# Optimization experiments

Measured on AMD Instinct MI355X. Metric: run time of the kernel, lower is better.

The kernel has to match this reference:

```python
import jax, jax.numpy as jnp
import numpy as np

L, D, H, M, NC = 12, 768, 12, 3072, 1000
P, IMG, C = 16, 224, 3
HD = D // H // 2  # 32: diff-attn head dim (2*H query heads of HD, H value heads of 2*HD)
B = 32
N = (IMG // P) ** 2 + 1  # 197
EPS = 1e-5


def _layernorm(x, s, b):
    mu = x.mean(-1, keepdims=True)
    var = ((x - mu) ** 2).mean(-1, keepdims=True)
    return (x - mu) * jax.lax.rsqrt(var + EPS) * s + b


def _rmsnorm(x, s):
    ms = (x * x).mean(-1, keepdims=True)
    return x * jax.lax.rsqrt(ms + EPS) * s


def _diff_attn(x, qw, kw, vw, ow, lq1, lk1, lq2, lk2, sls, lam_init):
    b, n, _ = x.shape
    q = (x @ qw).reshape(b, n, 2 * H, HD)
    k = (x @ kw).reshape(b, n, 2 * H, HD)
    v = (x @ vw).reshape(b, n, H, 2 * HD)
    scores = jnp.einsum('bnhd,bmhd->bhnm', q, k) * (HD ** -0.5)
    attn = jax.nn.softmax(scores, axis=-1)  # [b, 2H, n, n]
    lam = jnp.exp(jnp.sum(lq1 * lk1)) - jnp.exp(jnp.sum(lq2 * lk2)) + lam_init
    attn = attn.reshape(b, H, 2, n, n)
    attn = attn[:, :, 0] - lam * attn[:, :, 1]  # differential attention map
    out = jnp.einsum('bhnm,bmhd->bnhd', attn, v)  # [b, n, H, 2*HD]
    out = _rmsnorm(out, sls) * (1.0 - lam_init)
    return out.reshape(b, n, D) @ ow


def _forward(x, conv_w, conv_b, cls_token, pos_emb,
             ln1_s, ln1_b, q_w, k_w, v_w, o_w, lq1, lk1, lq2, lk2, subln_s,
             ln2_s, ln2_b, w1, b1, w2, b2, lnf_s, lnf_b, head_w, head_b):
    # patch embed: conv stride=patch, then flatten to tokens
    h = jax.lax.conv_general_dilated(x, conv_w, (P, P), 'VALID',
                                     dimension_numbers=('NCHW', 'OIHW', 'NCHW'))
    h = h + conv_b[None, :, None, None]
    bsz = x.shape[0]
    h = h.reshape(bsz, D, -1).transpose(0, 2, 1)  # [B, 196, D]
    h = jnp.concatenate([jnp.broadcast_to(cls_token, (bsz, 1, D)), h], axis=1)
    h = h + pos_emb
    for i in range(L):
        lam_init = 0.8 - 0.6 * np.exp(-0.3 * i)
        a = _diff_attn(_layernorm(h, ln1_s[i], ln1_b[i]), q_w[i], k_w[i], v_w[i], o_w[i],
                       lq1[i], lk1[i], lq2[i], lk2[i], subln_s[i], lam_init)
        h = h + a
        m = _layernorm(h, ln2_s[i], ln2_b[i])
        m = jax.nn.gelu(m @ w1[i] + b1[i]) @ w2[i] + b2[i]
        h = h + m
    h = _layernorm(h, lnf_s, lnf_b)
    return h[:, 0] @ head_w + head_b


def setup_inputs() -> dict:
    key = jax.random.key(0)
    ks = iter(jax.random.split(key, 40))
    def rn(shape, s=0.02):
        return jax.random.normal(next(ks), shape, jnp.float32) * s
    return {
        'x': jax.random.normal(next(ks), (B, C, IMG, IMG), jnp.float32),
        'conv_w': rn((D, C, P, P)), 'conv_b': jnp.zeros((D,), jnp.float32),
        'cls_token': jnp.zeros((1, 1, D), jnp.float32),
        'pos_emb': rn((1, N, D)),
        'ln1_s': jnp.ones((L, D), jnp.float32), 'ln1_b': jnp.zeros((L, D), jnp.float32),
        'q_w': rn((L, D, D)), 'k_w': rn((L, D, D)), 'v_w': rn((L, D, D)), 'o_w': rn((L, D, D)),
        'lq1': rn((L, HD), 0.1), 'lk1': rn((L, HD), 0.1),
        'lq2': rn((L, HD), 0.1), 'lk2': rn((L, HD), 0.1),
        'subln_s': jnp.ones((L, 2 * HD), jnp.float32),
        'ln2_s': jnp.ones((L, D), jnp.float32), 'ln2_b': jnp.zeros((L, D), jnp.float32),
        'w1': rn((L, D, M)), 'b1': jnp.zeros((L, M), jnp.float32),
        'w2': rn((L, M, D)), 'b2': jnp.zeros((L, D), jnp.float32),
        'lnf_s': jnp.ones((D,), jnp.float32), 'lnf_b': jnp.zeros((D,), jnp.float32),
        'head_w': rn((D, NC)), 'head_b': jnp.zeros((NC,), jnp.float32),
    }


def reference(x, conv_w, conv_b, cls_token, pos_emb,
              ln1_s, ln1_b, q_w, k_w, v_w, o_w, lq1, lk1, lq2, lk2, subln_s,
              ln2_s, ln2_b, w1, b1, w2, b2, lnf_s, lnf_b, head_w, head_b):
    return _forward(x, conv_w, conv_b, cls_token, pos_emb,
                    ln1_s, ln1_b, q_w, k_w, v_w, o_w, lq1, lk1, lq2, lk2, subln_s,
                    ln2_s, ln2_b, w1, b1, w2, b2, lnf_s, lnf_b, head_w, head_b)
```

## Files before the change

### kernel.cpp

```cpp
#include <hip/hip_runtime.h>
#include <cmath>


typedef unsigned short u16;
typedef u16 u16x4 __attribute__((ext_vector_type(4)));
typedef u16 u16x8 __attribute__((ext_vector_type(8)));
typedef float fx4 __attribute__((ext_vector_type(4)));
typedef __bf16 bf16x8 __attribute__((ext_vector_type(8)));

#define MROWS 6304
#define MPAD  6400

#define WAITV(N) asm volatile("s_waitcnt vmcnt(" #N ")" ::: "memory")

__device__ __forceinline__ float bf2f(u16 u) {
  union { unsigned int i; float f; } c; c.i = ((unsigned int)u) << 16; return c.f;
}
__device__ __forceinline__ u16 f2bf(float f) {
  union { float f; unsigned int i; } c; c.f = f;
  return (u16)((c.i + 0x7FFFu + ((c.i >> 16) & 1u)) >> 16);
}
__device__ __forceinline__ float gelu_f(float x) {
  float u = 0.7978845608028654f * (x + 0.044715f * x * x * x);
  u = fminf(fmaxf(u, -30.f), 30.f);
  float e = __expf(2.f * u);
  return 0.5f * x * (1.f + (e - 1.f) / (e + 1.f));
}

__device__ __forceinline__ void gload16(const void* g, void* l) {
  __builtin_amdgcn_global_load_lds(
      (const __attribute__((address_space(1))) void*)g,
      (__attribute__((address_space(3))) void*)l, 16, 0, 0);
}

__device__ __forceinline__ int xcd_swz(int orig, int nwg) {
  int q = nwg >> 3, r = nwg & 7;
  int x = orig & 7, i = orig >> 3;
  return (x < r ? x * (q + 1) : r * (q + 1) + (x - r) * q) + i;
}

enum { EP_F32 = 0, EP_BF16 = 1, EP_GELU_BF16 = 2, EP_RESID_F32 = 3 };

template<int MODE>
__device__ __forceinline__ void ep_store(void* outp, const float* __restrict__ resid,
                                         size_t m, size_t n, size_t N, float v) {
  if (MODE == EP_GELU_BF16)      ((u16*)outp)[m * N + n] = f2bf(gelu_f(v));
  else if (MODE == EP_BF16)      ((u16*)outp)[m * N + n] = f2bf(v);
  else if (MODE == EP_RESID_F32) ((float*)outp)[m * N + n] = resid[m * N + n] + v;
  else                           ((float*)outp)[m * N + n] = v;
}

template<int MODE, bool BIAS>
__device__ __forceinline__
void gemm_256_body(const u16* __restrict__ A, const u16* __restrict__ Bt,
                   const float* __restrict__ bias, const float* __restrict__ resid,
                   void* __restrict__ outp, int M, int N, int K, int NT)
{
  extern __shared__ unsigned char lds[];
  const int tid = threadIdx.x;
  const int lane = tid & 63, w = tid >> 6;
  const int g = lane >> 4, l = lane & 15;
  const int wr = w >> 2, wc = w & 3;
  const int wg = xcd_swz(blockIdx.x, gridDim.x);
  const int bm = (wg / NT) * 256, bn = (wg % NT) * 256;
  const int NKT = K >> 6;

  const int srow = w * 16 + (lane >> 3);
  const int scol = ((lane & 7) ^ ((lane >> 3) & 7)) << 3;
  const u16* gA = A + (size_t)bm * K + scol;
  const u16* gB = Bt + (size_t)bn * K + scol;
  const int ldso = (w * 16) * 128;

  auto STG = [&](int buf, int op, int half, int t) {
    const u16* src = (op ? gB : gA) + (size_t)(half * 128 + srow) * K + t * 64;
    unsigned char* d = lds + buf * 65536 + op * 32768 + half * 16384 + ldso;
    gload16(src, d);
    gload16(src + (size_t)8 * K, d + 1024);
  };

  fx4 acc[2][2][4][2] = {};

  STG(0, 0, 0, 0); STG(0, 1, 0, 0); STG(0, 0, 1, 0); STG(0, 1, 1, 0);
  STG(1, 0, 0, 1); STG(1, 1, 0, 1);
  WAITV(4);
  __builtin_amdgcn_s_barrier();

  for (int T = 0; T < NKT; ++T) {
    const unsigned char* Ab = lds + (T & 1) * 65536;
    const unsigned char* Bb = Ab + 32768;

#define RD_A(i2, kk, mh) (*(const bf16x8*)(Ab + ((mh)*128 + wr*64 + (i2)*16 + l)*128 + (((kk)*64 + g*16) ^ ((l & 7) << 4))))
#define RD_B(j2, kk, nh) (*(const bf16x8*)(Bb + ((nh)*128 + wc*32 + (j2)*16 + l)*128 + (((kk)*64 + g*16) ^ ((l & 7) << 4))))
#define PHASE(mh, nh, DOWAIT, ...)                                             \
    {                                                                          \
      bf16x8 af0[4], af1[4], bq0[2], bq1[2];                                   \
      _Pragma("unroll") for (int i2 = 0; i2 < 4; ++i2) {                       \
        af0[i2] = RD_A(i2, 0, mh); af1[i2] = RD_A(i2, 1, mh);                  \
      }                                                                        \
      _Pragma("unroll") for (int j2 = 0; j2 < 2; ++j2) {                       \
        bq0[j2] = RD_B(j2, 0, nh); bq1[j2] = RD_B(j2, 1, nh);                  \
      }                                                                        \
      __VA_ARGS__;                                                             \
      if (DOWAIT) WAITV(4);                                                    \
      __builtin_amdgcn_s_barrier();                                            \
      asm volatile("s_waitcnt lgkmcnt(0)" ::: "memory");                       \
      __builtin_amdgcn_sched_barrier(0);                                       \
      __builtin_amdgcn_s_setprio(1);                                           \
      _Pragma("unroll") for (int i2 = 0; i2 < 4; ++i2)                         \
        _Pragma("unroll") for (int j2 = 0; j2 < 2; ++j2) {                     \
          acc[mh][nh][i2][j2] = __builtin_amdgcn_mfma_f32_16x16x32_bf16(       \
              af0[i2], bq0[j2], acc[mh][nh][i2][j2], 0, 0, 0);                 \
          acc[mh][nh][i2][j2] = __builtin_amdgcn_mfma_f32_16x16x32_bf16(       \
              af1[i2], bq1[j2], acc[mh][nh][i2][j2], 0, 0, 0);                 \
        }                                                                      \
      __builtin_amdgcn_s_setprio(0);                                           \
      __builtin_amdgcn_s_barrier();                                            \
    }

    PHASE(0, 0, false, { if (T + 1 < NKT) STG((T + 1) & 1, 0, 1, T + 1); })
    PHASE(0, 1, false, { if (T + 1 < NKT) STG((T + 1) & 1, 1, 1, T + 1); })
    PHASE(1, 0, false, { if (T + 2 < NKT) STG(T & 1, 0, 0, T + 2); })
    PHASE(1, 1, true,  { if (T + 2 < NKT) STG(T & 1, 1, 0, T + 2); })

#undef PHASE
#undef RD_A
#undef RD_B
  }

  #pragma unroll
  for (int mh = 0; mh < 2; ++mh)
    #pragma unroll
    for (int i2 = 0; i2 < 4; ++i2)
      #pragma unroll
      for (int qr = 0; qr < 4; ++qr) {
        int m = bm + mh * 128 + wr * 64 + i2 * 16 + g * 4 + qr;
        if (m < M) {
          #pragma unroll
          for (int nh = 0; nh < 2; ++nh)
            #pragma unroll
            for (int j2 = 0; j2 < 2; ++j2) {
              int n = bn + nh * 128 + wc * 32 + j2 * 16 + l;
              float bv = BIAS ? bias[n] : 0.f;
              ep_store<MODE>(outp, resid, m, n, N, acc[mh][nh][i2][j2][qr] + bv);
            }
        }
      }
}

template<int MODE, bool BIAS>
__device__ __forceinline__
void gemm_n64_body(const u16* __restrict__ A, const u16* __restrict__ Bt,
                   const float* __restrict__ bias, const float* __restrict__ resid,
                   void* __restrict__ outp, int M, int N, int K, int NT)
{
  __shared__ unsigned char lds[2][(128 + 64) * 64 * 2];
  const int tid = threadIdx.x;
  const int lane = tid & 63, w = tid >> 6;
  const int g = lane >> 4, l = lane & 15;
  const int wg = xcd_swz(blockIdx.x, gridDim.x);
  const int bm = (wg / NT) * 128, bn = (wg % NT) * 64;

  const int swz_half = ((lane & 7) ^ ((lane >> 3) & 7)) << 3;
  const u16* gA = A + (size_t)(bm + 32 * w + (lane >> 3)) * K + swz_half;
  const u16* gB = Bt + (size_t)(bn + 16 * w + (lane >> 3)) * K + swz_half;

  fx4 acc[2][4] = {};

  auto STAGE = [&](int buf, int kt) {
    unsigned char* bA = &lds[buf][0] + 4096 * w;
    unsigned char* bB = &lds[buf][0] + 16384 + 2048 * w;
    #pragma unroll
    for (int c = 0; c < 4; ++c)
      gload16(gA + (size_t)(8 * c) * K + kt, bA + (8 * c) * 128);
    #pragma unroll
    for (int c = 0; c < 2; ++c)
      gload16(gB + (size_t)(8 * c) * K + kt, bB + (8 * c) * 128);
  };

  STAGE(0, 0);
  int cur = 0;
  for (int kt = 0; kt < K; kt += 64) {
    if (kt + 64 < K) {
      STAGE(cur ^ 1, kt + 64);
      WAITV(6);
    } else {
      WAITV(0);
    }
    __builtin_amdgcn_s_barrier();
    __builtin_amdgcn_sched_barrier(0);
    const unsigned char* As = &lds[cur][0];
    const unsigned char* Bs = As + 16384;
    #pragma unroll
    for (int kk = 0; kk < 2; ++kk) {
      bf16x8 af[2], bfr[4];
      #pragma unroll
      for (int i = 0; i < 2; ++i) {
        int ar = w * 32 + i * 16 + l;
        af[i] = *(const bf16x8*)(As + ar * 128 + ((kk * 64 + g * 16) ^ ((ar & 7) << 4)));
      }
      #pragma unroll
      for (int j = 0; j < 4; ++j) {
        int br = j * 16 + l;
        bfr[j] = *(const bf16x8*)(Bs + br * 128 + ((kk * 64 + g * 16) ^ ((br & 7) << 4)));
      }
      #pragma unroll
      for (int i = 0; i < 2; ++i)
        #pragma unroll
        for (int j = 0; j < 4; ++j)
          acc[i][j] = __builtin_amdgcn_mfma_f32_16x16x32_bf16(af[i], bfr[j], acc[i][j], 0, 0, 0);
    }
    __builtin_amdgcn_sched_barrier(0);
    __builtin_amdgcn_s_barrier();
    cur ^= 1;
  }
  #pragma unroll
  for (int j = 0; j < 4; ++j) {
    int n = bn + j * 16 + l;
    float bv = BIAS ? bias[n] : 0.f;
    #pragma unroll
    for (int i = 0; i < 2; ++i) {
      int mbase = bm + w * 32 + i * 16 + g * 4;
      #pragma unroll
      for (int q = 0; q < 4; ++q) {
        int m = mbase + q;
        if (m < M) ep_store<MODE>(outp, resid, m, n, N, acc[i][j][q] + bv);
      }
    }
  }
}

__global__ __launch_bounds__(256) void patch_gemm(const u16* A, const u16* Bt, float* outp) {
  gemm_n64_body<EP_F32, false>(A, Bt, nullptr, nullptr, outp, 6272, 768, 768, 12);
}
__global__ __launch_bounds__(512) void qkv_gemm(const u16* A, const u16* Bt, u16* outp) {
  gemm_256_body<EP_BF16, false>(A, Bt, nullptr, nullptr, outp, MROWS, 2304, 768, 9);
}
__global__ __launch_bounds__(256) void oproj_gemm(const u16* A, const u16* Bt,
                                                  const float* resid, float* outp) {
  gemm_n64_body<EP_RESID_F32, false>(A, Bt, nullptr, resid, outp, MROWS, 768, 768, 12);
}
__global__ __launch_bounds__(512) void mlp1_gemm(const u16* A, const u16* Bt,
                                                 const float* bias, u16* outp) {
  gemm_256_body<EP_GELU_BF16, true>(A, Bt, bias, nullptr, outp, MROWS, 3072, 768, 12);
}
__global__ __launch_bounds__(256) void mlp2_gemm(const u16* A, const u16* Bt,
                                                 const float* bias, const float* resid,
                                                 float* outp) {
  gemm_n64_body<EP_RESID_F32, true>(A, Bt, bias, resid, outp, MROWS, 768, 3072, 12);
}

template<bool OUTF32>
__global__ __launch_bounds__(64)
void layernorm_k(const float* __restrict__ x, const float* __restrict__ s,
                 const float* __restrict__ b, void* __restrict__ outp, size_t in_rstride)
{
  int r = blockIdx.x, lane = threadIdx.x;
  const fx4* xp = (const fx4*)(x + (size_t)r * in_rstride);
  fx4 v[3];
  float sum = 0.f, sq = 0.f;
  #pragma unroll
  for (int j = 0; j < 3; ++j) {
    v[j] = xp[j * 64 + lane];
    #pragma unroll
    for (int e = 0; e < 4; ++e) { sum += v[j][e]; sq += v[j][e] * v[j][e]; }
  }
  #pragma unroll
  for (int off = 32; off; off >>= 1) { sum += __shfl_xor(sum, off); sq += __shfl_xor(sq, off); }
  float mu = sum * (1.f / 768.f);
  float var = sq * (1.f / 768.f) - mu * mu;
  float rs = rsqrtf(var + 1e-5f);
  const fx4* sp = (const fx4*)s;
  const fx4* bp = (const fx4*)b;
  #pragma unroll
  for (int j = 0; j < 3; ++j) {
    fx4 sv = sp[j * 64 + lane], bv = bp[j * 64 + lane];
    if (OUTF32) {
      fx4 o;
      #pragma unroll
      for (int e = 0; e < 4; ++e) o[e] = (v[j][e] - mu) * rs * sv[e] + bv[e];
      *(fx4*)((float*)outp + (size_t)r * 768 + (j * 64 + lane) * 4) = o;
    } else {
      u16x4 o;
      #pragma unroll
      for (int e = 0; e < 4; ++e) o[e] = f2bf((v[j][e] - mu) * rs * sv[e] + bv[e]);
      *(u16x4*)((u16*)outp + (size_t)r * 768 + (j * 64 + lane) * 4) = o;
    }
  }
}

#define KSTR 40
#define VSTR 232
#define DA_LDS (2 * 224 * KSTR * 2 + 64 * VSTR * 2 + 4 * 16 * VSTR * 2)

__global__ __launch_bounds__(256)
void diff_attn(const u16* __restrict__ qkv, const float* __restrict__ lam_p,
               const float* __restrict__ sls, u16* __restrict__ outp, float lam_init)
{
  extern __shared__ char smem[];
  u16* K1s = (u16*)smem;
  u16* K2s = K1s + 224 * KSTR;
  u16* Vt  = K2s + 224 * KSTR;
  const int tid = threadIdx.x;
  const int w = tid >> 6, lane = tid & 63;
  const int g = lane >> 4, l = lane & 15;
  u16* Pw = Vt + 64 * VSTR + w * 16 * VSTR;

  const int bh = blockIdx.x;
  const int b = bh / 12, hh = bh % 12;
  const u16* base = qkv + (size_t)b * 197 * 2304;

  if (tid < 197) {
    const u16* kr = base + (size_t)tid * 2304 + 768 + hh * 64;
    *(u16x8*)(K1s + tid * KSTR + 0)  = *(const u16x8*)(kr + 0);
    *(u16x8*)(K1s + tid * KSTR + 8)  = *(const u16x8*)(kr + 8);
    *(u16x8*)(K1s + tid * KSTR + 16) = *(const u16x8*)(kr + 16);
    *(u16x8*)(K1s + tid * KSTR + 24) = *(const u16x8*)(kr + 24);
    *(u16x8*)(K2s + tid * KSTR + 0)  = *(const u16x8*)(kr + 32);
    *(u16x8*)(K2s + tid * KSTR + 8)  = *(const u16x8*)(kr + 40);
    *(u16x8*)(K2s + tid * KSTR + 16) = *(const u16x8*)(kr + 48);
    *(u16x8*)(K2s + tid * KSTR + 24) = *(const u16x8*)(kr + 56);
    const u16* vr = base + (size_t)tid * 2304 + 1536 + hh * 64;
    #pragma unroll
    for (int jj = 0; jj < 8; ++jj) {
      u16x8 vv = *(const u16x8*)(vr + jj * 8);
      #pragma unroll
      for (int e = 0; e < 8; ++e) Vt[(jj * 8 + e) * VSTR + tid] = vv[e];
    }
  }
  for (int idx = tid; idx < 64 * 27; idx += 256) {
    Vt[(idx / 27) * VSTR + 197 + (idx % 27)] = 0;
  }
  __syncthreads();

  const float lam = lam_p[0];
  const float oscale = 1.f - lam_init;
  const float scale = 0.17677669529663687f;
  const fx4 zero = {};

  for (int qb = w; qb < 13; qb += 4) {
    const int qbase = qb * 16;
    const u16* qrow = base + (size_t)(qbase + l) * 2304 + hh * 64;
    bf16x8 qf1 = *(const bf16x8*)(qrow + g * 8);
    bf16x8 qf2 = *(const bf16x8*)(qrow + 32 + g * 8);

    fx4 s1[14], s2[14];
    #pragma unroll
    for (int t = 0; t < 14; ++t) {
      bf16x8 kf1 = *(const bf16x8*)(K1s + (t * 16 + l) * KSTR + g * 8);
      bf16x8 kf2 = *(const bf16x8*)(K2s + (t * 16 + l) * KSTR + g * 8);
      s1[t] = __builtin_amdgcn_mfma_f32_16x16x32_bf16(qf1, kf1, zero, 0, 0, 0);
      s2[t] = __builtin_amdgcn_mfma_f32_16x16x32_bf16(qf2, kf2, zero, 0, 0, 0);
    }

    float mx1[4] = {-1e30f, -1e30f, -1e30f, -1e30f};
    float mx2[4] = {-1e30f, -1e30f, -1e30f, -1e30f};
    #pragma unroll
    for (int t = 0; t < 14; ++t) {
      bool ok = (t * 16 + l) < 197;
      #pragma unroll
      for (int q = 0; q < 4; ++q) {
        float v1 = ok ? s1[t][q] * scale : -1e30f;
        float v2 = ok ? s2[t][q] * scale : -1e30f;
        s1[t][q] = v1; s2[t][q] = v2;
        mx1[q] = fmaxf(mx1[q], v1); mx2[q] = fmaxf(mx2[q], v2);
      }
    }
    #pragma unroll
    for (int off = 8; off; off >>= 1)
      #pragma unroll
      for (int q = 0; q < 4; ++q) {
        mx1[q] = fmaxf(mx1[q], __shfl_xor(mx1[q], off));
        mx2[q] = fmaxf(mx2[q], __shfl_xor(mx2[q], off));
      }
    float z1[4] = {0, 0, 0, 0}, z2[4] = {0, 0, 0, 0};
    #pragma unroll
    for (int t = 0; t < 14; ++t)
      #pragma unroll
      for (int q = 0; q < 4; ++q) {
        float p1 = __expf(s1[t][q] - mx1[q]);
        float p2 = __expf(s2[t][q] - mx2[q]);
        s1[t][q] = p1; s2[t][q] = p2;
        z1[q] += p1; z2[q] += p2;
      }
    #pragma unroll
    for (int off = 8; off; off >>= 1)
      #pragma unroll
      for (int q = 0; q < 4; ++q) {
        z1[q] += __shfl_xor(z1[q], off);
        z2[q] += __shfl_xor(z2[q], off);
      }
    float r1[4], r2[4];
    #pragma unroll
    for (int q = 0; q < 4; ++q) { r1[q] = 1.f / z1[q]; r2[q] = lam / z2[q]; }

    #pragma unroll
    for (int t = 0; t < 14; ++t)
      #pragma unroll
      for (int q = 0; q < 4; ++q) {
        float pc = s1[t][q] * r1[q] - s2[t][q] * r2[q];
        Pw[(g * 4 + q) * VSTR + t * 16 + l] = f2bf(pc);
      }

    fx4 o[4] = {};
    #pragma unroll
    for (int mt = 0; mt < 7; ++mt) {
      bf16x8 pa = *(const bf16x8*)(Pw + l * VSTR + mt * 32 + g * 8);
      #pragma unroll
      for (int j = 0; j < 4; ++j) {
        bf16x8 vb = *(const bf16x8*)(Vt + (j * 16 + l) * VSTR + mt * 32 + g * 8);
        o[j] = __builtin_amdgcn_mfma_f32_16x16x32_bf16(pa, vb, o[j], 0, 0, 0);
      }
    }

    float ms[4] = {0, 0, 0, 0};
    #pragma unroll
    for (int j = 0; j < 4; ++j)
      #pragma unroll
      for (int q = 0; q < 4; ++q) ms[q] += o[j][q] * o[j][q];
    #pragma unroll
    for (int off = 8; off; off >>= 1)
      #pragma unroll
      for (int q = 0; q < 4; ++q) ms[q] += __shfl_xor(ms[q], off);
    float rr[4];
    #pragma unroll
    for (int q = 0; q < 4; ++q) rr[q] = rsqrtf(ms[q] * (1.f / 64.f) + 1e-5f) * oscale;
    #pragma unroll
    for (int j = 0; j < 4; ++j) {
      float slv = sls[j * 16 + l];
      #pragma unroll
      for (int q = 0; q < 4; ++q) {
        int row = qbase + g * 4 + q;
        if (row < 197)
          outp[(size_t)(b * 197 + row) * 768 + hh * 64 + j * 16 + l] = f2bf(o[j][q] * rr[q] * slv);
      }
    }
  }
}

__global__ __launch_bounds__(256)
void prep_weights(const float* __restrict__ qw, const float* __restrict__ kw,
                  const float* __restrict__ vw, const float* __restrict__ ow,
                  const float* __restrict__ w1, const float* __restrict__ w2,
                  u16* __restrict__ qkvt, u16* __restrict__ ot,
                  u16* __restrict__ w1t, u16* __restrict__ w2t,
                  const float* __restrict__ lq1, const float* __restrict__ lk1,
                  const float* __restrict__ lq2, const float* __restrict__ lk2,
                  float* __restrict__ lam_out, float lam_init)
{
  int bid = blockIdx.x;
  if (bid == 1728) {
    if (threadIdx.x < 64) {
      int lane = threadIdx.x;
      float p1 = lane < 32 ? lq1[lane] * lk1[lane] : 0.f;
      float p2 = lane < 32 ? lq2[lane] * lk2[lane] : 0.f;
      #pragma unroll
      for (int off = 32; off; off >>= 1) { p1 += __shfl_xor(p1, off); p2 += __shfl_xor(p2, off); }
      if (lane == 0) lam_out[0] = __expf(p1) - __expf(p2) + lam_init;
    }
    return;
  }
  const float* src; u16* dst; int Kd, Nd, tx, ty;
  if (bid < 576) {
    int which = bid / 144, t = bid % 144;
    ty = t / 12; tx = t % 12; Kd = 768; Nd = 768;
    src = (which == 0) ? qw : (which == 1) ? kw : (which == 2) ? vw : ow;
    dst = (which < 3) ? (qkvt + (size_t)which * 768 * 768) : ot;
  } else if (bid < 1152) {
    int t = bid - 576; ty = t / 12; tx = t % 12; Kd = 768; Nd = 3072; src = w1; dst = w1t;
  } else {
    int t = bid - 1152; ty = t / 48; tx = t % 48; Kd = 3072; Nd = 768; src = w2; dst = w2t;
  }
  __shared__ u16 tile[64][65];
  int tid2 = threadIdx.x;
  int k0 = tx * 64, n0 = ty * 64;
  #pragma unroll
  for (int j = 0; j < 16; ++j) {
    int idx = j * 256 + tid2;
    int rr = idx >> 6, cc = idx & 63;
    tile[rr][cc] = f2bf(src[(size_t)(k0 + rr) * Nd + n0 + cc]);
  }
  __syncthreads();
  #pragma unroll
  for (int j = 0; j < 16; ++j) {
    int idx = j * 256 + tid2;
    int rr = idx >> 6, cc = idx & 63;
    dst[(size_t)(n0 + rr) * Kd + k0 + cc] = tile[cc][rr];
  }
}

__global__ void convert_cw(const float* __restrict__ src, u16* __restrict__ dst)
{
  int i4 = blockIdx.x * 256 + threadIdx.x;
  fx4 v = *(const fx4*)(src + (size_t)i4 * 4);
  u16x4 o;
  #pragma unroll
  for (int e = 0; e < 4; ++e) o[e] = f2bf(v[e]);
  *(u16x4*)(dst + (size_t)i4 * 4) = o;
}

__global__ void im2col(const float* __restrict__ x, u16* __restrict__ A0)
{
  int i4 = blockIdx.x * 256 + threadIdx.x;
  int base = i4 * 4;
  int r = base / 768, c0 = base % 768;
  int b = r / 196, p = r % 196;
  int py = p / 14, px = p % 14;
  int ch = c0 >> 8;
  int cc = c0 & 255;
  int iy = cc >> 4, ix = cc & 15;
  const float* src = x + (((size_t)(b * 3 + ch) * 224 + py * 16 + iy) * 224 + px * 16 + ix);
  fx4 v = *(const fx4*)src;
  u16x4 o;
  #pragma unroll
  for (int e = 0; e < 4; ++e) o[e] = f2bf(v[e]);
  *(u16x4*)(A0 + base) = o;
}

__global__ void assemble(const float* __restrict__ tmp, const float* __restrict__ conv_b,
                         const float* __restrict__ cls, const float* __restrict__ pos,
                         float* __restrict__ h)
{
  int i4 = blockIdx.x * 256 + threadIdx.x;
  int base = i4 * 4;
  int r = base / 768, d = base % 768;
  int b = r / 197, n = r % 197;
  fx4 pv = *(const fx4*)(pos + (size_t)n * 768 + d);
  fx4 v;
  if (n == 0) {
    v = *(const fx4*)(cls + d);
  } else {
    v = *(const fx4*)(tmp + (size_t)(b * 196 + n - 1) * 768 + d);
    fx4 cb = *(const fx4*)(conv_b + d);
    v = v + cb;
  }
  *(fx4*)(h + (size_t)r * 768 + d) = v + pv;
}

__global__ __launch_bounds__(256)
void head_kernel(const float* __restrict__ ln, const float* __restrict__ hw,
                 const float* __restrict__ hb, float* __restrict__ outp)
{
  int r = blockIdx.x;
  int c = blockIdx.y * 256 + threadIdx.x;
  if (c >= 1000) return;
  const float* lr = ln + (size_t)r * 768;
  float acc = hb[c];
  for (int d = 0; d < 768; ++d)
    acc = fmaf(lr[d], hw[(size_t)d * 1000 + c], acc);
  outp[r * 1000 + c] = acc;
}

extern "C" void kernel_launch(void* const* d_in, const int* in_sizes, int n_in,
                              void* d_out, int out_size, void* d_ws, size_t ws_size,
                              hipStream_t stream)
{
  (void)in_sizes; (void)n_in; (void)out_size; (void)ws_size;
  const float* x      = (const float*)d_in[0];
  const float* conv_w = (const float*)d_in[1];
  const float* conv_b = (const float*)d_in[2];
  const float* cls    = (const float*)d_in[3];
  const float* pos    = (const float*)d_in[4];
  const float* ln1_s  = (const float*)d_in[5];
  const float* ln1_b  = (const float*)d_in[6];
  const float* q_w    = (const float*)d_in[7];
  const float* k_w    = (const float*)d_in[8];
  const float* v_w    = (const float*)d_in[9];
  const float* o_w    = (const float*)d_in[10];
  const float* lq1    = (const float*)d_in[11];
  const float* lk1    = (const float*)d_in[12];
  const float* lq2    = (const float*)d_in[13];
  const float* lk2    = (const float*)d_in[14];
  const float* slsx   = (const float*)d_in[15];
  const float* ln2_s  = (const float*)d_in[16];
  const float* ln2_b  = (const float*)d_in[17];
  const float* w1     = (const float*)d_in[18];
  const float* b1     = (const float*)d_in[19];
  const float* w2     = (const float*)d_in[20];
  const float* b2     = (const float*)d_in[21];
  const float* lnf_s  = (const float*)d_in[22];
  const float* lnf_b  = (const float*)d_in[23];
  const float* head_w = (const float*)d_in[24];
  const float* head_b = (const float*)d_in[25];
  float* out = (float*)d_out;

  char* ws = (char*)d_ws;
  size_t off = 0;
  auto alloc = [&](size_t bytes) { size_t p = off; off += (bytes + 255) & ~(size_t)255; return p; };
  u16*   A_bf  = (u16*)  (ws + alloc((size_t)MPAD * 768 * 2));
  u16*   big   = (u16*)  (ws + alloc((size_t)MPAD * 3072 * 2));
  float* h     = (float*)(ws + alloc((size_t)MROWS * 768 * 4));
  u16*   wqkv  = (u16*)  (ws + alloc((size_t)2304 * 768 * 2));
  u16*   wo    = (u16*)  (ws + alloc((size_t)768 * 768 * 2));
  u16*   w1t   = (u16*)  (ws + alloc((size_t)3072 * 768 * 2));
  u16*   w2t   = (u16*)  (ws + alloc((size_t)768 * 3072 * 2));
  float* lnf_o = (float*)(ws + alloc((size_t)32 * 768 * 4));
  float* lam   = (float*)(ws + alloc(256));
  float* convtmp = (float*)big;
  u16*   cwbf  = w1t;

  hipFuncSetAttribute((const void*)diff_attn,
                      hipFuncAttributeMaxDynamicSharedMemorySize, DA_LDS);
  hipFuncSetAttribute((const void*)qkv_gemm,
                      hipFuncAttributeMaxDynamicSharedMemorySize, 131072);
  hipFuncSetAttribute((const void*)mlp1_gemm,
                      hipFuncAttributeMaxDynamicSharedMemorySize, 131072);

  convert_cw<<<576, 256, 0, stream>>>(conv_w, cwbf);
  im2col<<<4704, 256, 0, stream>>>(x, A_bf);
  patch_gemm<<<588, 256, 0, stream>>>(A_bf, cwbf, convtmp);
  assemble<<<4728, 256, 0, stream>>>(convtmp, conv_b, cls, pos, h);

  for (int l = 0; l < 12; ++l) {
    float lam_init = 0.8f - 0.6f * expf(-0.3f * (float)l);
    prep_weights<<<1729, 256, 0, stream>>>(
        q_w + (size_t)l * 589824, k_w + (size_t)l * 589824,
        v_w + (size_t)l * 589824, o_w + (size_t)l * 589824,
        w1 + (size_t)l * 2359296, w2 + (size_t)l * 2359296,
        wqkv, wo, w1t, w2t,
        lq1 + l * 32, lk1 + l * 32, lq2 + l * 32, lk2 + l * 32,
        lam, lam_init);
    layernorm_k<false><<<MROWS, 64, 0, stream>>>(h, ln1_s + l * 768, ln1_b + l * 768, A_bf, (size_t)768);
    qkv_gemm<<<225, 512, 131072, stream>>>(A_bf, wqkv, big);
    diff_attn<<<384, 256, DA_LDS, stream>>>(big, lam, slsx + l * 64, A_bf, lam_init);
    oproj_gemm<<<600, 256, 0, stream>>>(A_bf, wo, h, h);
    layernorm_k<false><<<MROWS, 64, 0, stream>>>(h, ln2_s + l * 768, ln2_b + l * 768, A_bf, (size_t)768);
    mlp1_gemm<<<300, 512, 131072, stream>>>(A_bf, w1t, b1 + l * 3072, big);
    mlp2_gemm<<<600, 256, 0, stream>>>(big, w2t, b2 + l * 768, h, h);
  }

  layernorm_k<true><<<32, 64, 0, stream>>>(h, lnf_s, lnf_b, lnf_o, (size_t)197 * 768);
  head_kernel<<<dim3(32, 4), 256, 0, stream>>>(lnf_o, head_w, head_b, out);
}
```

Before: 3.136 ms.

## Triple-buffer N64 GEMM loads and retile MLP1 into 128x128 blocks

The N=64 GEMM body (patch, o-proj, mlp2) moves from a double-buffered static LDS pipeline to a triple-buffered one in dynamic LDS, so loads run two k-tiles ahead with matching vmcnt waits. MLP1 drops the 256x256, 512-thread kernel for a new 128x128, 256-thread tiled kernel launched over 1200 workgroups. The aim is to hide global-load latency better and raise occupancy and grid balance for MLP1. In exchange, the smaller MLP1 tiles get less reuse per workgroup, and the N64 kernels use more LDS per workgroup.

```diff
diff --git a/kernel.cpp b/kernel.cpp
--- a/kernel.cpp
+++ b/kernel.cpp
@@ -149,16 +149,97 @@
 
 template<int MODE, bool BIAS>
 __device__ __forceinline__
+void gemm_big_body(const u16* __restrict__ A, const u16* __restrict__ Bt,
+                   const float* __restrict__ bias, const float* __restrict__ resid,
+                   void* __restrict__ outp, int M, int N, int K, int NT)
+{
+  __shared__ unsigned char lds[2][2 * 128 * 64 * 2];
+  const int tid = threadIdx.x;
+  const int lane = tid & 63, w = tid >> 6;
+  const int g = lane >> 4, l = lane & 15;
+  const int wr = w >> 1, wc = w & 1;
+  const int wg = xcd_swz(blockIdx.x, gridDim.x);
+  const int bm = (wg / NT) * 128, bn = (wg % NT) * 128;
+
+  const int swz_half = ((lane & 7) ^ ((lane >> 3) & 7)) << 3;
+  const int srow = 32 * w + (lane >> 3);
+  const u16* gA = A + (size_t)(bm + srow) * K + swz_half;
+  const u16* gB = Bt + (size_t)(bn + srow) * K + swz_half;
+
+  fx4 acc[4][4] = {};
+
+  auto STAGE = [&](int buf, int kt) {
+    unsigned char* bA = &lds[buf][0] + 4096 * w;
+    unsigned char* bB = bA + 16384;
+    #pragma unroll
+    for (int c = 0; c < 4; ++c) {
+      gload16(gA + (size_t)(8 * c) * K + kt, bA + (8 * c) * 128);
+      gload16(gB + (size_t)(8 * c) * K + kt, bB + (8 * c) * 128);
+    }
+  };
+
+  STAGE(0, 0);
+  int cur = 0;
+  for (int kt = 0; kt < K; kt += 64) {
+    if (kt + 64 < K) {
+      STAGE(cur ^ 1, kt + 64);
+      WAITV(8);
+    } else {
+      WAITV(0);
+    }
+    __builtin_amdgcn_s_barrier();
+    __builtin_amdgcn_sched_barrier(0);
+    const unsigned char* As = &lds[cur][0];
+    const unsigned char* Bs = As + 16384;
+    #pragma unroll
+    for (int kk = 0; kk < 2; ++kk) {
+      bf16x8 af[4], bfr[4];
+      #pragma unroll
+      for (int i = 0; i < 4; ++i) {
+        int ar = wr * 64 + i * 16 + l;
+        af[i] = *(const bf16x8*)(As + ar * 128 + ((kk * 64 + g * 16) ^ ((ar & 7) << 4)));
+        int br = wc * 64 + i * 16 + l;
+        bfr[i] = *(const bf16x8*)(Bs + br * 128 + ((kk * 64 + g * 16) ^ ((br & 7) << 4)));
+      }
+      #pragma unroll
+      for (int i = 0; i < 4; ++i)
+        #pragma unroll
+        for (int j = 0; j < 4; ++j)
+          acc[i][j] = __builtin_amdgcn_mfma_f32_16x16x32_bf16(af[i], bfr[j], acc[i][j], 0, 0, 0);
+    }
+    __builtin_amdgcn_sched_barrier(0);
+    __builtin_amdgcn_s_barrier();
+    cur ^= 1;
+  }
+  #pragma unroll
+  for (int j = 0; j < 4; ++j) {
+    int n = bn + wc * 64 + j * 16 + l;
+    float bv = BIAS ? bias[n] : 0.f;
+    #pragma unroll
+    for (int i = 0; i < 4; ++i) {
+      int mbase = bm + wr * 64 + i * 16 + g * 4;
+      #pragma unroll
+      for (int q = 0; q < 4; ++q) {
+        int m = mbase + q;
+        if (m < M) ep_store<MODE>(outp, resid, m, n, N, acc[i][j][q] + bv);
+      }
+    }
+  }
+}
+
+template<int MODE, bool BIAS>
+__device__ __forceinline__
 void gemm_n64_body(const u16* __restrict__ A, const u16* __restrict__ Bt,
                    const float* __restrict__ bias, const float* __restrict__ resid,
                    void* __restrict__ outp, int M, int N, int K, int NT)
 {
-  __shared__ unsigned char lds[2][(128 + 64) * 64 * 2];
+  extern __shared__ unsigned char lds3[];
   const int tid = threadIdx.x;
   const int lane = tid & 63, w = tid >> 6;
   const int g = lane >> 4, l = lane & 15;
   const int wg = xcd_swz(blockIdx.x, gridDim.x);
   const int bm = (wg / NT) * 128, bn = (wg % NT) * 64;
+  const int NKT = K >> 6;
 
   const int swz_half = ((lane & 7) ^ ((lane >> 3) & 7)) << 3;
   const u16* gA = A + (size_t)(bm + 32 * w + (lane >> 3)) * K + swz_half;
@@ -166,29 +247,32 @@
 
   fx4 acc[2][4] = {};
 
-  auto STAGE = [&](int buf, int kt) {
-    unsigned char* bA = &lds[buf][0] + 4096 * w;
-    unsigned char* bB = &lds[buf][0] + 16384 + 2048 * w;
+  auto STAGE = [&](int buf, int t) {
+    unsigned char* bA = lds3 + buf * 24576 + 4096 * w;
+    unsigned char* bB = lds3 + buf * 24576 + 16384 + 2048 * w;
     #pragma unroll
     for (int c = 0; c < 4; ++c)
-      gload16(gA + (size_t)(8 * c) * K + kt, bA + (8 * c) * 128);
+      gload16(gA + (size_t)(8 * c) * K + t * 64, bA + (8 * c) * 128);
     #pragma unroll
     for (int c = 0; c < 2; ++c)
-      gload16(gB + (size_t)(8 * c) * K + kt, bB + (8 * c) * 128);
+      gload16(gB + (size_t)(8 * c) * K + t * 64, bB + (8 * c) * 128);
   };
 
   STAGE(0, 0);
-  int cur = 0;
-  for (int kt = 0; kt < K; kt += 64) {
-    if (kt + 64 < K) {
-      STAGE(cur ^ 1, kt + 64);
+  if (NKT > 1) STAGE(1, 1);
+  int bufc = 0, bufs = 2;
+  for (int T = 0; T < NKT; ++T) {
+    if (T + 2 < NKT) {
+      STAGE(bufs, T + 2);
+      WAITV(12);
+    } else if (T + 1 < NKT) {
       WAITV(6);
     } else {
       WAITV(0);
     }
     __builtin_amdgcn_s_barrier();
     __builtin_amdgcn_sched_barrier(0);
-    const unsigned char* As = &lds[cur][0];
+    const unsigned char* As = lds3 + bufc * 24576;
     const unsigned char* Bs = As + 16384;
     #pragma unroll
     for (int kk = 0; kk < 2; ++kk) {
@@ -211,7 +295,8 @@
     }
     __builtin_amdgcn_sched_barrier(0);
     __builtin_amdgcn_s_barrier();
-    cur ^= 1;
+    bufc = (bufc == 2) ? 0 : bufc + 1;
+    bufs = (bufs == 2) ? 0 : bufs + 1;
   }
   #pragma unroll
   for (int j = 0; j < 4; ++j) {
@@ -229,6 +314,8 @@
   }
 }
 
+#define N64_LDS (3 * 24576)
+
 __global__ __launch_bounds__(256) void patch_gemm(const u16* A, const u16* Bt, float* outp) {
   gemm_n64_body<EP_F32, false>(A, Bt, nullptr, nullptr, outp, 6272, 768, 768, 12);
 }
@@ -239,9 +326,9 @@
                                                   const float* resid, float* outp) {
   gemm_n64_body<EP_RESID_F32, false>(A, Bt, nullptr, resid, outp, MROWS, 768, 768, 12);
 }
-__global__ __launch_bounds__(512) void mlp1_gemm(const u16* A, const u16* Bt,
+__global__ __launch_bounds__(256) void mlp1_gemm(const u16* A, const u16* Bt,
                                                  const float* bias, u16* outp) {
-  gemm_256_body<EP_GELU_BF16, true>(A, Bt, bias, nullptr, outp, MROWS, 3072, 768, 12);
+  gemm_big_body<EP_GELU_BF16, true>(A, Bt, bias, nullptr, outp, MROWS, 3072, 768, 24);
 }
 __global__ __launch_bounds__(256) void mlp2_gemm(const u16* A, const u16* Bt,
                                                  const float* bias, const float* resid,
@@ -602,12 +689,16 @@
                       hipFuncAttributeMaxDynamicSharedMemorySize, DA_LDS);
   hipFuncSetAttribute((const void*)qkv_gemm,
                       hipFuncAttributeMaxDynamicSharedMemorySize, 131072);
-  hipFuncSetAttribute((const void*)mlp1_gemm,
-                      hipFuncAttributeMaxDynamicSharedMemorySize, 131072);
+  hipFuncSetAttribute((const void*)patch_gemm,
+                      hipFuncAttributeMaxDynamicSharedMemorySize, N64_LDS);
+  hipFuncSetAttribute((const void*)oproj_gemm,
+                      hipFuncAttributeMaxDynamicSharedMemorySize, N64_LDS);
+  hipFuncSetAttribute((const void*)mlp2_gemm,
+                      hipFuncAttributeMaxDynamicSharedMemorySize, N64_LDS);
 
   convert_cw<<<576, 256, 0, stream>>>(conv_w, cwbf);
   im2col<<<4704, 256, 0, stream>>>(x, A_bf);
-  patch_gemm<<<588, 256, 0, stream>>>(A_bf, cwbf, convtmp);
+  patch_gemm<<<588, 256, N64_LDS, stream>>>(A_bf, cwbf, convtmp);
   assemble<<<4728, 256, 0, stream>>>(convtmp, conv_b, cls, pos, h);
 
   for (int l = 0; l < 12; ++l) {
@@ -622,10 +713,10 @@
     layernorm_k<false><<<MROWS, 64, 0, stream>>>(h, ln1_s + l * 768, ln1_b + l * 768, A_bf, (size_t)768);
     qkv_gemm<<<225, 512, 131072, stream>>>(A_bf, wqkv, big);
     diff_attn<<<384, 256, DA_LDS, stream>>>(big, lam, slsx + l * 64, A_bf, lam_init);
-    oproj_gemm<<<600, 256, 0, stream>>>(A_bf, wo, h, h);
+    oproj_gemm<<<600, 256, N64_LDS, stream>>>(A_bf, wo, h, h);
     layernorm_k<false><<<MROWS, 64, 0, stream>>>(h, ln2_s + l * 768, ln2_b + l * 768, A_bf, (size_t)768);
-    mlp1_gemm<<<300, 512, 131072, stream>>>(A_bf, w1t, b1 + l * 3072, big);
-    mlp2_gemm<<<600, 256, 0, stream>>>(big, w2t, b2 + l * 768, h, h);
+    mlp1_gemm<<<1200, 256, 0, stream>>>(A_bf, w1t, b1 + l * 3072, big);
+    mlp2_gemm<<<600, 256, N64_LDS, stream>>>(big, w2t, b2 + l * 768, h, h);
   }
 
   layernorm_k<true><<<32, 64, 0, stream>>>(h, lnf_s, lnf_b, lnf_o, (size_t)197 * 768);
```

Result: slower. 3.397 ms (+8.3%).
